# Kernel optimization log

Measured on AMD Instinct MI355X. Metric: run time of the kernel, lower is better.

## Reference

```python
import jax, jax.numpy as jnp
import numpy as np

PHI = (1.0 + 5.0 ** 0.5) / 2.0
_VS = np.array([[-1, PHI, 0], [1, PHI, 0], [-1, -PHI, 0], [1, -PHI, 0],
                [0, -1, PHI], [0, 1, PHI], [0, -1, -PHI], [0, 1, -PHI],
                [PHI, 0, -1], [PHI, 0, 1], [-PHI, 0, -1], [-PHI, 0, 1]], dtype=np.float32)
_FACES = np.array([(1, 2, 7), (1, 3, 7), (1, 3, 5), (1, 4, 5), (1, 2, 4), (2, 7, 8), (3, 7, 9),
                   (3, 5, 11), (4, 5, 6), (2, 4, 10), (2, 8, 10), (7, 8, 9), (3, 9, 11),
                   (5, 6, 11), (4, 6, 10), (0, 8, 10), (0, 6, 10), (0, 6, 11), (0, 9, 11), (0, 8, 9)])
_fn = _VS[_FACES].sum(1)
_fn = _fn / np.linalg.norm(_fn, axis=-1, keepdims=True)
FACE_NORMAL = jnp.asarray(_fn, dtype=jnp.float32)  # (20, 3)
_FTC = np.array([(1, 4, 0, 2, 3), (2, 0, 1, 4, 3), (3, 1, 0, 4, 2), (4, 2, 0, 3, 1), (0, 3, 1, 2, 4),
                 (3, 2, 0, 4, 1), (4, 3, 0, 2, 1), (0, 4, 1, 2, 3), (1, 0, 2, 4, 3), (2, 1, 0, 4, 3),
                 (4, 0, 1, 3, 2), (0, 1, 2, 3, 4), (1, 2, 0, 3, 4), (2, 3, 0, 1, 4), (3, 4, 0, 1, 2),
                 (1, 3, 0, 2, 4), (0, 2, 1, 3, 4), (4, 1, 0, 3, 2), (3, 0, 1, 4, 2), (2, 4, 0, 1, 3)])
# each row of _FTC is a permutation of 0..4; scatter_(-1, ftc, W) == gather with the inverse perm
INV_FTC = jnp.asarray(np.argsort(_FTC, axis=-1))                 # (20, 5)
M_COLOR = jnp.asarray(np.eye(5, dtype=np.float32)[_FTC[:, 0]])   # (20, 5) one-hot scatter-add matrix
ROLL = jnp.asarray(np.array([(0, 1, 2, 3, 4), (0, 1, 3, 4, 2), (0, 1, 4, 2, 3)]))


def _build_kernel(w19):
    """(..., 19) -> (..., 9, 20, 5): build 9 symmetric kernel rows, then apply the
    per-face permutation (equivalent to the original zeros_like + scatter_)."""
    rep3 = lambda x: jnp.repeat(x, 3, axis=-1)
    top = jnp.concatenate([w19[..., 0:2], rep3(w19[..., 2:3])], -1)[..., None, :]
    bottom = jnp.concatenate([w19[..., 3:5], rep3(w19[..., 5:6])], -1)[..., None, :]
    center = jnp.concatenate([w19[..., 6:8], rep3(w19[..., 8:9])], -1)[..., None, :]
    sym = w19[..., 9:19].reshape(w19.shape[:-1] + (2, 5))
    sym = sym[..., ROLL].reshape(w19.shape[:-1] + (6, 5))
    w9 = jnp.concatenate([top, bottom, sym, center], axis=-2)     # (..., 9, 5)
    return jnp.take(w9, INV_FTC, axis=-1)                          # (..., 9, 20, 5)


def setup_inputs() -> dict:
    key = jax.random.key(0)
    k1, k2, k3, k4 = jax.random.split(key, 4)
    B, V, N, CIN, COUT = 2, 10000, 16, 128, 64
    stdv = 1.0 / np.sqrt(COUT * 6)
    return {
        "neighbor_index": jax.random.randint(k1, (B, V, N), 0, V, dtype=jnp.int32),
        "vertices": jax.random.normal(k2, (B, V, 3), jnp.float32),
        "W": jax.random.uniform(k3, (COUT, CIN, 19), jnp.float32, -stdv, stdv),
        "W_dir": jax.random.uniform(k4, (CIN, 19), jnp.float32, -stdv, stdv),
    }


def reference(neighbor_index, vertices, W, W_dir):
    # gather neighbor positions: (b, q, n, 3)
    neighbors = jax.vmap(lambda v, i: v[i])(vertices, neighbor_index)
    d = neighbors - vertices[:, :, None, :]
    d = d / jnp.maximum(jnp.linalg.norm(d, axis=-1, keepdims=True), 1e-12)  # F.normalize
    # project onto 20 face normals, tanh, scatter-add to 5 colors
    de = jnp.tanh(jnp.einsum('fi,bqni->bqnf', FACE_NORMAL, d))             # (b,q,n,20)
    de5 = jnp.einsum('bqnf,fs->bqns', de, M_COLOR)                         # (b,q,n,5)
    # torch einsum broadcast of size-1 c dim == contraction after summing weights over c
    wd = _build_kernel(W_dir).sum(0)                                       # (9,20,5)
    act = jax.nn.relu(jnp.einsum('kri,bqni->bkqnr', wd, de5))              # (b,9,q,n,20)
    nfm = jnp.einsum('bkqnr,bqni->bkqir', act, de5)                        # (b,9,q,5,20)
    ws = _build_kernel(W).sum(1)                                           # (d_out,9,20,5)
    ka = jnp.einsum('dkri,bkqir->bdqr', ws, nfm)                           # (b,d_out,q,20)
    return jnp.einsum('bdqr,rs->bdqs', ka, M_COLOR)                        # (b,d_out,q,5)
```

## Files before the change

### kernel.cpp

```cpp
#include <hip/hip_runtime.h>
#include <math.h>

#define V_CNT 10000
#define NB 16
#define TQ 16
#define BQ_TOTAL 20000

#define WS_W45T  0
#define WS_WD9   2880
#define WS_FN    2944

#define PST 84

__device__ __constant__ int FTC_d[20][5] = {
  {1,4,0,2,3},{2,0,1,4,3},{3,1,0,4,2},{4,2,0,3,1},{0,3,1,2,4},
  {3,2,0,4,1},{4,3,0,2,1},{0,4,1,2,3},{1,0,2,4,3},{2,1,0,4,3},
  {4,0,1,3,2},{0,1,2,3,4},{1,2,0,3,4},{2,3,0,1,4},{3,4,0,1,2},
  {1,3,0,2,4},{0,2,1,3,4},{4,1,0,3,2},{3,0,1,4,2},{2,4,0,1,3}};

__device__ __constant__ int RBYCOL_d[5][4] = {
  {4,7,11,16},{0,8,12,15},{1,9,13,19},{2,5,14,18},{3,6,10,17}};

constexpr int COLF[20] = {1,2,3,4,0,3,4,0,1,2,4,0,1,2,3,1,0,4,3,2};

constexpr int W9MAP[9][5] = {
  {0,1,2,2,2},{3,4,5,5,5},
  {9,10,11,12,13},{9,10,12,13,11},{9,10,13,11,12},
  {14,15,16,17,18},{14,15,17,18,16},{14,15,18,16,17},
  {6,7,8,8,8}};

__device__ __constant__ int FACES_d[20][3] = {
  {1,2,7},{1,3,7},{1,3,5},{1,4,5},{1,2,4},{2,7,8},{3,7,9},{3,5,11},{4,5,6},{2,4,10},
  {2,8,10},{7,8,9},{3,9,11},{5,6,11},{4,6,10},{0,8,10},{0,6,10},{0,6,11},{0,9,11},{0,8,9}};

#define PHI_F 1.61803398874989484820f
__device__ __constant__ float VS_d[12][3] = {
  {-1.f,PHI_F,0.f},{1.f,PHI_F,0.f},{-1.f,-PHI_F,0.f},{1.f,-PHI_F,0.f},
  {0.f,-1.f,PHI_F},{0.f,1.f,PHI_F},{0.f,-1.f,-PHI_F},{0.f,1.f,-PHI_F},
  {PHI_F,0.f,-1.f},{PHI_F,0.f,1.f},{-PHI_F,0.f,-1.f},{-PHI_F,0.f,1.f}};

__device__ __forceinline__ float fast_tanh(float x){
  float e = __expf(2.0f * x);
  return 1.0f - 2.0f * __builtin_amdgcn_rcpf(e + 1.0f);
}

__global__ __launch_bounds__(128) void prep_kernel(const float* __restrict__ W,
                                                   const float* __restrict__ Wdir,
                                                   float* __restrict__ ws){
  __shared__ float buf[128][20];
  __shared__ float w19s[19];
  int d = blockIdx.x;
  int c = threadIdx.x;

  const float* src = (d < 64) ? (W + ((size_t)d*128 + c)*19) : (Wdir + (size_t)c*19);
  #pragma unroll
  for (int tt = 0; tt < 19; ++tt) buf[c][tt] = src[tt];

  if (d == 64 && c < 20){
    float x=0.f, y=0.f, z=0.f;
    #pragma unroll
    for (int vv=0; vv<3; ++vv){
      int vi = FACES_d[c][vv];
      x += VS_d[vi][0]; y += VS_d[vi][1]; z += VS_d[vi][2];
    }
    float inv = rsqrtf(x*x + y*y + z*z);
    ws[WS_FN + c*3 + 0] = x*inv;
    ws[WS_FN + c*3 + 1] = y*inv;
    ws[WS_FN + c*3 + 2] = z*inv;
  }
  __syncthreads();

  if (c < 19){
    float s = 0.f;
    for (int i = 0; i < 128; ++i) s += buf[i][c];
    w19s[c] = s;
  }
  __syncthreads();

  if (c < 45){
    int k = c / 5, j = c % 5;
    float v = w19s[W9MAP[k][j]];
    if (d < 64) ws[WS_W45T + c*64 + d] = v;
    else        ws[WS_WD9  + c]        = v;
  }
}

__global__ __launch_bounds__(320) void fold_kernel(const int*   __restrict__ nbr,
                                                   const float* __restrict__ verts,
                                                   const float* __restrict__ ws,
                                                   float* __restrict__ out){
  __shared__ float de5s[TQ][NB][5];
  __shared__ float Ps2T[45][PST];
  __shared__ float W45T[45][64];
  int t = threadIdx.x;
  int blockq0 = blockIdx.x * TQ;

  {
    float* wl = &W45T[0][0];
    #pragma unroll
    for (int sW = 0; sW < 9; ++sW) wl[t + sW*320] = ws[WS_W45T + t + sW*320];
  }

  if (t < TQ*NB){
    int ql = t >> 4;
    int n  = t & 15;
    int qg = blockq0 + ql;
    int q  = (qg >= V_CNT) ? (qg - V_CNT) : qg;
    int b0 = qg - q;
    int idx = nbr[qg*NB + n];
    float vx = verts[qg*3+0], vy = verts[qg*3+1], vz = verts[qg*3+2];
    const float* nv = verts + (size_t)(b0 + idx)*3;
    float dx = nv[0]-vx, dy = nv[1]-vy, dz = nv[2]-vz;
    float dd = dx*dx + dy*dy + dz*dz;
    float inv = (dd > 0.f) ? rsqrtf(dd) : 0.f;
    dx *= inv; dy *= inv; dz *= inv;
    const float* fnp = ws + WS_FN;
    float s0=0.f, s1=0.f, s2=0.f, s3=0.f, s4=0.f;
    #pragma unroll
    for (int f = 0; f < 20; ++f){
      float x = fnp[f*3+0]*dx + fnp[f*3+1]*dy + fnp[f*3+2]*dz;
      float th = fast_tanh(x);
      if      (COLF[f]==0) s0 += th;
      else if (COLF[f]==1) s1 += th;
      else if (COLF[f]==2) s2 += th;
      else if (COLF[f]==3) s3 += th;
      else                 s4 += th;
    }
    de5s[ql][n][0]=s0; de5s[ql][n][1]=s1; de5s[ql][n][2]=s2;
    de5s[ql][n][3]=s3; de5s[ql][n][4]=s4;
  }
  __syncthreads();

  {
    int ql = t / 20;
    int g  = t - ql*20;
    int s  = g >> 2;
    int m  = g & 3;
    int r  = RBYCOL_d[s][m];
    int f0 = FTC_d[r][0], f1 = FTC_d[r][1], f2 = FTC_d[r][2],
        f3 = FTC_d[r][3], f4 = FTC_d[r][4];
    const float* de = &de5s[ql][0][0];

    float wdl[45];
    #pragma unroll
    for (int i = 0; i < 45; ++i) wdl[i] = ws[WS_WD9 + i];
    float acc[45];
    #pragma unroll
    for (int i = 0; i < 45; ++i) acc[i] = 0.f;

    float ne0 = de[f0], ne1 = de[f1], ne2 = de[f2], ne3 = de[f3], ne4 = de[f4];
    #pragma unroll
    for (int n = 0; n < NB; ++n){
      float e0 = ne0, e1 = ne1, e2 = ne2, e3 = ne3, e4 = ne4;
      if (n < NB-1){
        const float* dn = de + (n+1)*5;
        ne0 = dn[f0]; ne1 = dn[f1]; ne2 = dn[f2]; ne3 = dn[f3]; ne4 = dn[f4];
      }
      float e234 = e2 + e3 + e4;
      #pragma unroll
      for (int k = 0; k < 9; ++k){
        float a;
        if (k == 0 || k == 1 || k == 8)
          a = wdl[k*5+0]*e0 + wdl[k*5+1]*e1 + wdl[k*5+2]*e234;
        else
          a = wdl[k*5+0]*e0 + wdl[k*5+1]*e1 + wdl[k*5+2]*e2
            + wdl[k*5+3]*e3 + wdl[k*5+4]*e4;
        a = fmaxf(a, 0.f);
        acc[k*5+0] += a * e0;
        acc[k*5+1] += a * e1;
        acc[k*5+2] += a * e2;
        acc[k*5+3] += a * e3;
        acc[k*5+4] += a * e4;
      }
    }
    #pragma unroll
    for (int i = 0; i < 45; ++i){
      acc[i] += __shfl_xor(acc[i], 1);
      acc[i] += __shfl_xor(acc[i], 2);
    }
    if (m == 0){
      int col = ql*5 + s;
      #pragma unroll
      for (int i = 0; i < 45; ++i) Ps2T[i][col] = acc[i];
    }
  }
  __syncthreads();

  {
    int dq = t / 20;
    int cq = t - dq*20;
    float a00=0,a01=0,a02=0,a03=0, a10=0,a11=0,a12=0,a13=0,
          a20=0,a21=0,a22=0,a23=0, a30=0,a31=0,a32=0,a33=0;
    #pragma unroll
    for (int kj = 0; kj < 45; ++kj){
      float4 w = *(const float4*)&W45T[kj][dq*4];
      float4 p = *(const float4*)&Ps2T[kj][cq*4];
      a00 += w.x*p.x; a01 += w.x*p.y; a02 += w.x*p.z; a03 += w.x*p.w;
      a10 += w.y*p.x; a11 += w.y*p.y; a12 += w.y*p.z; a13 += w.y*p.w;
      a20 += w.z*p.x; a21 += w.z*p.y; a22 += w.z*p.z; a23 += w.z*p.w;
      a30 += w.w*p.x; a31 += w.w*p.y; a32 += w.w*p.z; a33 += w.w*p.w;
    }
    int b   = (blockq0 >= V_CNT) ? 1 : 0;
    int lq0 = blockq0 - b*V_CNT;
    float* ob = out + (size_t)b*3200000 + (size_t)lq0*5 + cq*4;
    int d0 = dq*4;
    *(float4*)&ob[(size_t)(d0+0)*50000] = make_float4(a00,a01,a02,a03);
    *(float4*)&ob[(size_t)(d0+1)*50000] = make_float4(a10,a11,a12,a13);
    *(float4*)&ob[(size_t)(d0+2)*50000] = make_float4(a20,a21,a22,a23);
    *(float4*)&ob[(size_t)(d0+3)*50000] = make_float4(a30,a31,a32,a33);
  }
}

extern "C" void kernel_launch(void* const* d_in, const int* in_sizes, int n_in,
                              void* d_out, int out_size, void* d_ws, size_t ws_size,
                              hipStream_t stream){
  const int*   nbr   = (const int*)d_in[0];
  const float* verts = (const float*)d_in[1];
  const float* W     = (const float*)d_in[2];
  const float* Wdir  = (const float*)d_in[3];
  float* out = (float*)d_out;
  float* ws  = (float*)d_ws;

  hipLaunchKernelGGL(prep_kernel, dim3(65), dim3(128), 0, stream, W, Wdir, ws);
  hipLaunchKernelGGL(fold_kernel, dim3(BQ_TOTAL/TQ), dim3(320), 0, stream, nbr, verts, ws, out);
}
```

Measured before the change: 100.5 us.

## Halve queries per block and split neighbor loop across thread pairs

```diff
diff --git a/kernel.cpp b/kernel.cpp
--- a/kernel.cpp
+++ b/kernel.cpp
@@ -3,14 +3,15 @@
 
 #define V_CNT 10000
 #define NB 16
-#define TQ 16
+#define TQ 8
 #define BQ_TOTAL 20000
+
 
 #define WS_W45T  0
 #define WS_WD9   2880
 #define WS_FN    2944
 
-#define PST 84
+#define PST 44
 
 __device__ __constant__ int FTC_d[20][5] = {
   {1,4,0,2,3},{2,0,1,4,3},{3,1,0,4,2},{4,2,0,3,1},{0,3,1,2,4},
@@ -132,14 +133,16 @@
   __syncthreads();
 
   {
-    int ql = t / 20;
-    int g  = t - ql*20;
-    int s  = g >> 2;
-    int m  = g & 3;
-    int r  = RBYCOL_d[s][m];
+    int ql  = t / 40;
+    int rem = t - ql*40;
+    int s   = rem >> 3;
+    int sub = rem & 7;
+    int m   = sub >> 1;
+    int nh  = sub & 1;
+    int r   = RBYCOL_d[s][m];
     int f0 = FTC_d[r][0], f1 = FTC_d[r][1], f2 = FTC_d[r][2],
         f3 = FTC_d[r][3], f4 = FTC_d[r][4];
-    const float* de = &de5s[ql][0][0];
+    const float* de = &de5s[ql][nh*8][0];
 
     float wdl[45];
     #pragma unroll
@@ -150,9 +153,9 @@
 
     float ne0 = de[f0], ne1 = de[f1], ne2 = de[f2], ne3 = de[f3], ne4 = de[f4];
     #pragma unroll
-    for (int n = 0; n < NB; ++n){
+    for (int n = 0; n < 8; ++n){
       float e0 = ne0, e1 = ne1, e2 = ne2, e3 = ne3, e4 = ne4;
-      if (n < NB-1){
+      if (n < 7){
         const float* dn = de + (n+1)*5;
         ne0 = dn[f0]; ne1 = dn[f1]; ne2 = dn[f2]; ne3 = dn[f3]; ne4 = dn[f4];
       }
@@ -177,8 +180,9 @@
     for (int i = 0; i < 45; ++i){
       acc[i] += __shfl_xor(acc[i], 1);
       acc[i] += __shfl_xor(acc[i], 2);
-    }
-    if (m == 0){
+      acc[i] += __shfl_xor(acc[i], 4);
+    }
+    if (sub == 0){
       int col = ql*5 + s;
       #pragma unroll
       for (int i = 0; i < 45; ++i) Ps2T[i][col] = acc[i];
@@ -189,25 +193,24 @@
   {
     int dq = t / 20;
     int cq = t - dq*20;
-    float a00=0,a01=0,a02=0,a03=0, a10=0,a11=0,a12=0,a13=0,
-          a20=0,a21=0,a22=0,a23=0, a30=0,a31=0,a32=0,a33=0;
+    float a00=0,a01=0, a10=0,a11=0, a20=0,a21=0, a30=0,a31=0;
     #pragma unroll
     for (int kj = 0; kj < 45; ++kj){
       float4 w = *(const float4*)&W45T[kj][dq*4];
-      float4 p = *(const float4*)&Ps2T[kj][cq*4];
-      a00 += w.x*p.x; a01 += w.x*p.y; a02 += w.x*p.z; a03 += w.x*p.w;
-      a10 += w.y*p.x; a11 += w.y*p.y; a12 += w.y*p.z; a13 += w.y*p.w;
-      a20 += w.z*p.x; a21 += w.z*p.y; a22 += w.z*p.z; a23 += w.z*p.w;
-      a30 += w.w*p.x; a31 += w.w*p.y; a32 += w.w*p.z; a33 += w.w*p.w;
+      float2 p = *(const float2*)&Ps2T[kj][cq*2];
+      a00 += w.x*p.x; a01 += w.x*p.y;
+      a10 += w.y*p.x; a11 += w.y*p.y;
+      a20 += w.z*p.x; a21 += w.z*p.y;
+      a30 += w.w*p.x; a31 += w.w*p.y;
     }
     int b   = (blockq0 >= V_CNT) ? 1 : 0;
     int lq0 = blockq0 - b*V_CNT;
-    float* ob = out + (size_t)b*3200000 + (size_t)lq0*5 + cq*4;
+    float* ob = out + (size_t)b*3200000 + (size_t)lq0*5 + cq*2;
     int d0 = dq*4;
-    *(float4*)&ob[(size_t)(d0+0)*50000] = make_float4(a00,a01,a02,a03);
-    *(float4*)&ob[(size_t)(d0+1)*50000] = make_float4(a10,a11,a12,a13);
-    *(float4*)&ob[(size_t)(d0+2)*50000] = make_float4(a20,a21,a22,a23);
-    *(float4*)&ob[(size_t)(d0+3)*50000] = make_float4(a30,a31,a32,a33);
+    *(float2*)&ob[(size_t)(d0+0)*50000] = make_float2(a00,a01);
+    *(float2*)&ob[(size_t)(d0+1)*50000] = make_float2(a10,a11);
+    *(float2*)&ob[(size_t)(d0+2)*50000] = make_float2(a20,a21);
+    *(float2*)&ob[(size_t)(d0+3)*50000] = make_float2(a30,a31);
   }
 }
 
```

Measured after the change: 112.2 us. +11.7%, slower.

## Use packed f32x2 math, transposed de5 layout, CSE'd activations, 8x4 output tiles

Applied to the files above, without the earlier changes.

```diff
diff --git a/kernel.cpp b/kernel.cpp
--- a/kernel.cpp
+++ b/kernel.cpp
@@ -6,11 +6,12 @@
 #define TQ 16
 #define BQ_TOTAL 20000
 
+
 #define WS_W45T  0
 #define WS_WD9   2880
 #define WS_FN    2944
 
-#define PST 84
+typedef float f32x2 __attribute__((ext_vector_type(2)));
 
 __device__ __constant__ int FTC_d[20][5] = {
   {1,4,0,2,3},{2,0,1,4,3},{3,1,0,4,2},{4,2,0,3,1},{0,3,1,2,4},
@@ -89,8 +90,8 @@
                                                    const float* __restrict__ verts,
                                                    const float* __restrict__ ws,
                                                    float* __restrict__ out){
-  __shared__ float de5s[TQ][NB][5];
-  __shared__ float Ps2T[45][PST];
+  __shared__ float de5s[TQ][5][20];
+  __shared__ float Ps2T[45][80];
   __shared__ float W45T[45][64];
   int t = threadIdx.x;
   int blockq0 = blockIdx.x * TQ;
@@ -126,8 +127,8 @@
       else if (COLF[f]==3) s3 += th;
       else                 s4 += th;
     }
-    de5s[ql][n][0]=s0; de5s[ql][n][1]=s1; de5s[ql][n][2]=s2;
-    de5s[ql][n][3]=s3; de5s[ql][n][4]=s4;
+    de5s[ql][0][n]=s0; de5s[ql][1][n]=s1; de5s[ql][2][n]=s2;
+    de5s[ql][3][n]=s3; de5s[ql][4][n]=s4;
   }
   __syncthreads();
 
@@ -139,75 +140,106 @@
     int r  = RBYCOL_d[s][m];
     int f0 = FTC_d[r][0], f1 = FTC_d[r][1], f2 = FTC_d[r][2],
         f3 = FTC_d[r][3], f4 = FTC_d[r][4];
-    const float* de = &de5s[ql][0][0];
+
+    const f32x2* P0 = (const f32x2*)&de5s[ql][0][0] + f0*10;
+    const f32x2* P1 = (const f32x2*)&de5s[ql][0][0] + f1*10;
+    const f32x2* P2 = (const f32x2*)&de5s[ql][0][0] + f2*10;
+    const f32x2* P3 = (const f32x2*)&de5s[ql][0][0] + f3*10;
+    const f32x2* P4 = (const f32x2*)&de5s[ql][0][0] + f4*10;
 
     float wdl[45];
     #pragma unroll
     for (int i = 0; i < 45; ++i) wdl[i] = ws[WS_WD9 + i];
-    float acc[45];
-    #pragma unroll
-    for (int i = 0; i < 45; ++i) acc[i] = 0.f;
-
-    float ne0 = de[f0], ne1 = de[f1], ne2 = de[f2], ne3 = de[f3], ne4 = de[f4];
-    #pragma unroll
-    for (int n = 0; n < NB; ++n){
-      float e0 = ne0, e1 = ne1, e2 = ne2, e3 = ne3, e4 = ne4;
-      if (n < NB-1){
-        const float* dn = de + (n+1)*5;
-        ne0 = dn[f0]; ne1 = dn[f1]; ne2 = dn[f2]; ne3 = dn[f3]; ne4 = dn[f4];
+
+    f32x2 acc01[9], acc23[9];
+    float acc4[9];
+    #pragma unroll
+    for (int k = 0; k < 9; ++k){ acc01[k] = (f32x2)0.f; acc23[k] = (f32x2)0.f; acc4[k] = 0.f; }
+
+    #pragma unroll
+    for (int np = 0; np < 8; ++np){
+      f32x2 E0 = P0[np], E1 = P1[np], E2 = P2[np], E3 = P3[np], E4 = P4[np];
+      #pragma unroll
+      for (int h = 0; h < 2; ++h){
+        float e0 = (h==0)?E0.x:E0.y, e1 = (h==0)?E1.x:E1.y,
+              e2 = (h==0)?E2.x:E2.y, e3 = (h==0)?E3.x:E3.y,
+              e4 = (h==0)?E4.x:E4.y;
+        float e234 = e2 + e3 + e4;
+        float c1 = wdl[10]*e0 + wdl[11]*e1;
+        float c2 = wdl[25]*e0 + wdl[26]*e1;
+        float a[9];
+        a[0] = fmaxf(wdl[ 0]*e0 + wdl[ 1]*e1 + wdl[ 2]*e234, 0.f);
+        a[1] = fmaxf(wdl[ 5]*e0 + wdl[ 6]*e1 + wdl[ 7]*e234, 0.f);
+        a[2] = fmaxf(c1 + wdl[12]*e2 + wdl[13]*e3 + wdl[14]*e4, 0.f);
+        a[3] = fmaxf(c1 + wdl[17]*e2 + wdl[18]*e3 + wdl[19]*e4, 0.f);
+        a[4] = fmaxf(c1 + wdl[22]*e2 + wdl[23]*e3 + wdl[24]*e4, 0.f);
+        a[5] = fmaxf(c2 + wdl[27]*e2 + wdl[28]*e3 + wdl[29]*e4, 0.f);
+        a[6] = fmaxf(c2 + wdl[32]*e2 + wdl[33]*e3 + wdl[34]*e4, 0.f);
+        a[7] = fmaxf(c2 + wdl[37]*e2 + wdl[38]*e3 + wdl[39]*e4, 0.f);
+        a[8] = fmaxf(wdl[40]*e0 + wdl[41]*e1 + wdl[42]*e234, 0.f);
+        f32x2 e01; e01.x = e0; e01.y = e1;
+        f32x2 e23; e23.x = e2; e23.y = e3;
+        #pragma unroll
+        for (int k = 0; k < 9; ++k){
+          f32x2 av; av.x = a[k]; av.y = a[k];
+          acc01[k] += av * e01;
+          acc23[k] += av * e23;
+          acc4[k]  += a[k] * e4;
+        }
       }
-      float e234 = e2 + e3 + e4;
-      #pragma unroll
-      for (int k = 0; k < 9; ++k){
-        float a;
-        if (k == 0 || k == 1 || k == 8)
-          a = wdl[k*5+0]*e0 + wdl[k*5+1]*e1 + wdl[k*5+2]*e234;
-        else
-          a = wdl[k*5+0]*e0 + wdl[k*5+1]*e1 + wdl[k*5+2]*e2
-            + wdl[k*5+3]*e3 + wdl[k*5+4]*e4;
-        a = fmaxf(a, 0.f);
-        acc[k*5+0] += a * e0;
-        acc[k*5+1] += a * e1;
-        acc[k*5+2] += a * e2;
-        acc[k*5+3] += a * e3;
-        acc[k*5+4] += a * e4;
-      }
-    }
-    #pragma unroll
-    for (int i = 0; i < 45; ++i){
-      acc[i] += __shfl_xor(acc[i], 1);
-      acc[i] += __shfl_xor(acc[i], 2);
+    }
+    #pragma unroll
+    for (int k = 0; k < 9; ++k){
+      acc01[k].x += __shfl_xor(acc01[k].x, 1); acc01[k].x += __shfl_xor(acc01[k].x, 2);
+      acc01[k].y += __shfl_xor(acc01[k].y, 1); acc01[k].y += __shfl_xor(acc01[k].y, 2);
+      acc23[k].x += __shfl_xor(acc23[k].x, 1); acc23[k].x += __shfl_xor(acc23[k].x, 2);
+      acc23[k].y += __shfl_xor(acc23[k].y, 1); acc23[k].y += __shfl_xor(acc23[k].y, 2);
+      acc4[k]    += __shfl_xor(acc4[k],    1); acc4[k]    += __shfl_xor(acc4[k],    2);
     }
     if (m == 0){
       int col = ql*5 + s;
       #pragma unroll
-      for (int i = 0; i < 45; ++i) Ps2T[i][col] = acc[i];
-    }
-  }
-  __syncthreads();
-
-  {
+      for (int k = 0; k < 9; ++k){
+        Ps2T[k*5+0][col] = acc01[k].x;
+        Ps2T[k*5+1][col] = acc01[k].y;
+        Ps2T[k*5+2][col] = acc23[k].x;
+        Ps2T[k*5+3][col] = acc23[k].y;
+        Ps2T[k*5+4][col] = acc4[k];
+      }
+    }
+  }
+  __syncthreads();
+
+  if (t < 160){
     int dq = t / 20;
     int cq = t - dq*20;
-    float a00=0,a01=0,a02=0,a03=0, a10=0,a11=0,a12=0,a13=0,
-          a20=0,a21=0,a22=0,a23=0, a30=0,a31=0,a32=0,a33=0;
-    #pragma unroll
+    f32x2 acc[8][2];
+    #pragma unroll
+    for (int r = 0; r < 8; ++r){ acc[r][0] = (f32x2)0.f; acc[r][1] = (f32x2)0.f; }
+    #pragma unroll 5
     for (int kj = 0; kj < 45; ++kj){
-      float4 w = *(const float4*)&W45T[kj][dq*4];
-      float4 p = *(const float4*)&Ps2T[kj][cq*4];
-      a00 += w.x*p.x; a01 += w.x*p.y; a02 += w.x*p.z; a03 += w.x*p.w;
-      a10 += w.y*p.x; a11 += w.y*p.y; a12 += w.y*p.z; a13 += w.y*p.w;
-      a20 += w.z*p.x; a21 += w.z*p.y; a22 += w.z*p.z; a23 += w.z*p.w;
-      a30 += w.w*p.x; a31 += w.w*p.y; a32 += w.w*p.z; a33 += w.w*p.w;
+      float4 w0 = *(const float4*)&W45T[kj][dq*8];
+      float4 w1 = *(const float4*)&W45T[kj][dq*8+4];
+      float4 p  = *(const float4*)&Ps2T[kj][cq*4];
+      f32x2 p01; p01.x = p.x; p01.y = p.y;
+      f32x2 p23; p23.x = p.z; p23.y = p.w;
+      float wr[8] = {w0.x,w0.y,w0.z,w0.w, w1.x,w1.y,w1.z,w1.w};
+      #pragma unroll
+      for (int r = 0; r < 8; ++r){
+        f32x2 wv; wv.x = wr[r]; wv.y = wr[r];
+        acc[r][0] += wv * p01;
+        acc[r][1] += wv * p23;
+      }
     }
     int b   = (blockq0 >= V_CNT) ? 1 : 0;
     int lq0 = blockq0 - b*V_CNT;
     float* ob = out + (size_t)b*3200000 + (size_t)lq0*5 + cq*4;
-    int d0 = dq*4;
-    *(float4*)&ob[(size_t)(d0+0)*50000] = make_float4(a00,a01,a02,a03);
-    *(float4*)&ob[(size_t)(d0+1)*50000] = make_float4(a10,a11,a12,a13);
-    *(float4*)&ob[(size_t)(d0+2)*50000] = make_float4(a20,a21,a22,a23);
-    *(float4*)&ob[(size_t)(d0+3)*50000] = make_float4(a30,a31,a32,a33);
+    int d0 = dq*8;
+    #pragma unroll
+    for (int r = 0; r < 8; ++r){
+      *(float4*)&ob[(size_t)(d0+r)*50000] =
+        make_float4(acc[r][0].x, acc[r][0].y, acc[r][1].x, acc[r][1].y);
+    }
   }
 }
 
```

New measurement: 112.3 us. 1.12x slower.

## Split direction-kernel accumulation into two passes with packed FP32 math and transposed de5 layout

Applied to the files above, without the earlier changes.

```diff
diff --git a/kernel.cpp b/kernel.cpp
--- a/kernel.cpp
+++ b/kernel.cpp
@@ -6,11 +6,12 @@
 #define TQ 16
 #define BQ_TOTAL 20000
 
+
 #define WS_W45T  0
 #define WS_WD9   2880
 #define WS_FN    2944
 
-#define PST 84
+typedef float f32x2 __attribute__((ext_vector_type(2)));
 
 __device__ __constant__ int FTC_d[20][5] = {
   {1,4,0,2,3},{2,0,1,4,3},{3,1,0,4,2},{4,2,0,3,1},{0,3,1,2,4},
@@ -89,8 +90,8 @@
                                                    const float* __restrict__ verts,
                                                    const float* __restrict__ ws,
                                                    float* __restrict__ out){
-  __shared__ float de5s[TQ][NB][5];
-  __shared__ float Ps2T[45][PST];
+  __shared__ float de5s[TQ][5][20];
+  __shared__ float Ps2T[45][80];
   __shared__ float W45T[45][64];
   int t = threadIdx.x;
   int blockq0 = blockIdx.x * TQ;
@@ -126,8 +127,8 @@
       else if (COLF[f]==3) s3 += th;
       else                 s4 += th;
     }
-    de5s[ql][n][0]=s0; de5s[ql][n][1]=s1; de5s[ql][n][2]=s2;
-    de5s[ql][n][3]=s3; de5s[ql][n][4]=s4;
+    de5s[ql][0][n]=s0; de5s[ql][1][n]=s1; de5s[ql][2][n]=s2;
+    de5s[ql][3][n]=s3; de5s[ql][4][n]=s4;
   }
   __syncthreads();
 
@@ -139,49 +140,120 @@
     int r  = RBYCOL_d[s][m];
     int f0 = FTC_d[r][0], f1 = FTC_d[r][1], f2 = FTC_d[r][2],
         f3 = FTC_d[r][3], f4 = FTC_d[r][4];
-    const float* de = &de5s[ql][0][0];
+
+    const f32x2* P0 = (const f32x2*)&de5s[ql][0][0] + f0*10;
+    const f32x2* P1 = (const f32x2*)&de5s[ql][0][0] + f1*10;
+    const f32x2* P2 = (const f32x2*)&de5s[ql][0][0] + f2*10;
+    const f32x2* P3 = (const f32x2*)&de5s[ql][0][0] + f3*10;
+    const f32x2* P4 = (const f32x2*)&de5s[ql][0][0] + f4*10;
 
     float wdl[45];
     #pragma unroll
     for (int i = 0; i < 45; ++i) wdl[i] = ws[WS_WD9 + i];
-    float acc[45];
-    #pragma unroll
-    for (int i = 0; i < 45; ++i) acc[i] = 0.f;
-
-    float ne0 = de[f0], ne1 = de[f1], ne2 = de[f2], ne3 = de[f3], ne4 = de[f4];
-    #pragma unroll
-    for (int n = 0; n < NB; ++n){
-      float e0 = ne0, e1 = ne1, e2 = ne2, e3 = ne3, e4 = ne4;
-      if (n < NB-1){
-        const float* dn = de + (n+1)*5;
-        ne0 = dn[f0]; ne1 = dn[f1]; ne2 = dn[f2]; ne3 = dn[f3]; ne4 = dn[f4];
-      }
-      float e234 = e2 + e3 + e4;
-      #pragma unroll
-      for (int k = 0; k < 9; ++k){
-        float a;
-        if (k == 0 || k == 1 || k == 8)
-          a = wdl[k*5+0]*e0 + wdl[k*5+1]*e1 + wdl[k*5+2]*e234;
-        else
-          a = wdl[k*5+0]*e0 + wdl[k*5+1]*e1 + wdl[k*5+2]*e2
-            + wdl[k*5+3]*e3 + wdl[k*5+4]*e4;
-        a = fmaxf(a, 0.f);
-        acc[k*5+0] += a * e0;
-        acc[k*5+1] += a * e1;
-        acc[k*5+2] += a * e2;
-        acc[k*5+3] += a * e3;
-        acc[k*5+4] += a * e4;
-      }
-    }
-    #pragma unroll
-    for (int i = 0; i < 45; ++i){
-      acc[i] += __shfl_xor(acc[i], 1);
-      acc[i] += __shfl_xor(acc[i], 2);
-    }
-    if (m == 0){
-      int col = ql*5 + s;
-      #pragma unroll
-      for (int i = 0; i < 45; ++i) Ps2T[i][col] = acc[i];
+    int col = ql*5 + s;
+
+    {
+      f32x2 a01[5], a23[5]; float a4[5];
+      #pragma unroll
+      for (int k = 0; k < 5; ++k){ a01[k] = (f32x2)0.f; a23[k] = (f32x2)0.f; a4[k] = 0.f; }
+      #pragma unroll
+      for (int np = 0; np < 8; ++np){
+        f32x2 E0 = P0[np], E1 = P1[np], E2 = P2[np], E3 = P3[np], E4 = P4[np];
+        #pragma unroll
+        for (int h = 0; h < 2; ++h){
+          float e0 = (h==0)?E0.x:E0.y, e1 = (h==0)?E1.x:E1.y,
+                e2 = (h==0)?E2.x:E2.y, e3 = (h==0)?E3.x:E3.y,
+                e4 = (h==0)?E4.x:E4.y;
+          float e234 = e2 + e3 + e4;
+          float c1 = wdl[10]*e0 + wdl[11]*e1;
+          f32x2 e01; e01.x = e0; e01.y = e1;
+          f32x2 e23; e23.x = e2; e23.y = e3;
+          #pragma unroll
+          for (int k = 0; k < 5; ++k){
+            float a;
+            if      (k == 0) a = wdl[ 0]*e0 + wdl[ 1]*e1 + wdl[ 2]*e234;
+            else if (k == 1) a = wdl[ 5]*e0 + wdl[ 6]*e1 + wdl[ 7]*e234;
+            else if (k == 2) a = c1 + wdl[12]*e2 + wdl[13]*e3 + wdl[14]*e4;
+            else if (k == 3) a = c1 + wdl[17]*e2 + wdl[18]*e3 + wdl[19]*e4;
+            else             a = c1 + wdl[22]*e2 + wdl[23]*e3 + wdl[24]*e4;
+            a = fmaxf(a, 0.f);
+            f32x2 av; av.x = a; av.y = a;
+            a01[k] += av * e01;
+            a23[k] += av * e23;
+            a4[k]  += a * e4;
+          }
+        }
+      }
+      #pragma unroll
+      for (int k = 0; k < 5; ++k){
+        a01[k].x += __shfl_xor(a01[k].x,1); a01[k].x += __shfl_xor(a01[k].x,2);
+        a01[k].y += __shfl_xor(a01[k].y,1); a01[k].y += __shfl_xor(a01[k].y,2);
+        a23[k].x += __shfl_xor(a23[k].x,1); a23[k].x += __shfl_xor(a23[k].x,2);
+        a23[k].y += __shfl_xor(a23[k].y,1); a23[k].y += __shfl_xor(a23[k].y,2);
+        a4[k]    += __shfl_xor(a4[k],   1); a4[k]    += __shfl_xor(a4[k],   2);
+      }
+      if (m == 0){
+        #pragma unroll
+        for (int k = 0; k < 5; ++k){
+          Ps2T[k*5+0][col] = a01[k].x;
+          Ps2T[k*5+1][col] = a01[k].y;
+          Ps2T[k*5+2][col] = a23[k].x;
+          Ps2T[k*5+3][col] = a23[k].y;
+          Ps2T[k*5+4][col] = a4[k];
+        }
+      }
+    }
+    asm volatile("" ::: "memory");
+
+    {
+      f32x2 a01[4], a23[4]; float a4[4];
+      #pragma unroll
+      for (int k = 0; k < 4; ++k){ a01[k] = (f32x2)0.f; a23[k] = (f32x2)0.f; a4[k] = 0.f; }
+      #pragma unroll
+      for (int np = 0; np < 8; ++np){
+        f32x2 E0 = P0[np], E1 = P1[np], E2 = P2[np], E3 = P3[np], E4 = P4[np];
+        #pragma unroll
+        for (int h = 0; h < 2; ++h){
+          float e0 = (h==0)?E0.x:E0.y, e1 = (h==0)?E1.x:E1.y,
+                e2 = (h==0)?E2.x:E2.y, e3 = (h==0)?E3.x:E3.y,
+                e4 = (h==0)?E4.x:E4.y;
+          float e234 = e2 + e3 + e4;
+          float c2 = wdl[25]*e0 + wdl[26]*e1;
+          f32x2 e01; e01.x = e0; e01.y = e1;
+          f32x2 e23; e23.x = e2; e23.y = e3;
+          #pragma unroll
+          for (int k = 0; k < 4; ++k){
+            float a;
+            if      (k == 0) a = c2 + wdl[27]*e2 + wdl[28]*e3 + wdl[29]*e4;
+            else if (k == 1) a = c2 + wdl[32]*e2 + wdl[33]*e3 + wdl[34]*e4;
+            else if (k == 2) a = c2 + wdl[37]*e2 + wdl[38]*e3 + wdl[39]*e4;
+            else             a = wdl[40]*e0 + wdl[41]*e1 + wdl[42]*e234;
+            a = fmaxf(a, 0.f);
+            f32x2 av; av.x = a; av.y = a;
+            a01[k] += av * e01;
+            a23[k] += av * e23;
+            a4[k]  += a * e4;
+          }
+        }
+      }
+      #pragma unroll
+      for (int k = 0; k < 4; ++k){
+        a01[k].x += __shfl_xor(a01[k].x,1); a01[k].x += __shfl_xor(a01[k].x,2);
+        a01[k].y += __shfl_xor(a01[k].y,1); a01[k].y += __shfl_xor(a01[k].y,2);
+        a23[k].x += __shfl_xor(a23[k].x,1); a23[k].x += __shfl_xor(a23[k].x,2);
+        a23[k].y += __shfl_xor(a23[k].y,1); a23[k].y += __shfl_xor(a23[k].y,2);
+        a4[k]    += __shfl_xor(a4[k],   1); a4[k]    += __shfl_xor(a4[k],   2);
+      }
+      if (m == 0){
+        #pragma unroll
+        for (int k = 0; k < 4; ++k){
+          Ps2T[25+k*5+0][col] = a01[k].x;
+          Ps2T[25+k*5+1][col] = a01[k].y;
+          Ps2T[25+k*5+2][col] = a23[k].x;
+          Ps2T[25+k*5+3][col] = a23[k].y;
+          Ps2T[25+k*5+4][col] = a4[k];
+        }
+      }
     }
   }
   __syncthreads();
```

Measured after the change: 104.0 us. +3.5%, slower.
